# Performance work log

Hardware: AMD Instinct MI355X
Metric: run time of the kernel (lower is better)

## Reference

```python
import jax, jax.numpy as jnp
import numpy as np

B, E_DIM, N_EXP, EXP_SZ, N_TASKS, TOPK = 16384, 512, 16, 512, 2, 3
D_IN = 2 * E_DIM      # 1024
D_HID = 4 * E_DIM     # 2048
EPS = 1e-5


def _ln(x, g, b):
    mu = jnp.mean(x, axis=-1, keepdims=True)
    var = jnp.var(x, axis=-1, keepdims=True)
    return (x - mu) * jax.lax.rsqrt(var + EPS) * g + b


def setup_inputs() -> dict:
    key = jax.random.key(0)
    ks = jax.random.split(key, 24)
    def w(k, shape, fan_in):
        return jax.random.normal(k, shape, jnp.float32) * (1.0 / np.sqrt(fan_in))
    return {
        "emb_paper": jax.random.normal(ks[0], (B, E_DIM), jnp.float32),
        "emb_reviewer": jax.random.normal(ks[1], (B, E_DIM), jnp.float32),
        # interaction encoder
        "enc_W1": w(ks[2], (D_IN, D_HID), D_IN), "enc_b1": jnp.zeros((D_HID,), jnp.float32),
        "ln1_g": jnp.ones((D_HID,), jnp.float32), "ln1_b": jnp.zeros((D_HID,), jnp.float32),
        "enc_W2": w(ks[3], (D_HID, D_IN), D_HID), "enc_b2": jnp.zeros((D_IN,), jnp.float32),
        "ln2_g": jnp.ones((D_IN,), jnp.float32), "ln2_b": jnp.zeros((D_IN,), jnp.float32),
        # per-task gates (stacked over task axis)
        "gW1": w(ks[4], (N_TASKS, D_IN, 128), D_IN), "gb1": jnp.zeros((N_TASKS, 128), jnp.float32),
        "gW2": w(ks[5], (N_TASKS, 128, N_EXP), 128), "gb2": jnp.zeros((N_TASKS, N_EXP), jnp.float32),
        # stacked experts
        "We1": w(ks[6], (N_EXP, D_IN, EXP_SZ), D_IN), "be1": jnp.zeros((N_EXP, EXP_SZ), jnp.float32),
        "We2": w(ks[7], (N_EXP, EXP_SZ, EXP_SZ), EXP_SZ), "be2": jnp.zeros((N_EXP, EXP_SZ), jnp.float32),
        # per-task towers
        "tW1": w(ks[8], (N_TASKS, EXP_SZ, 256), EXP_SZ), "tb1": jnp.zeros((N_TASKS, 256), jnp.float32),
        "tW2": w(ks[9], (N_TASKS, 256, 128), 256), "tb2": jnp.zeros((N_TASKS, 128), jnp.float32),
        "tW3": w(ks[10], (N_TASKS, 128, 1), 128), "tb3": jnp.zeros((N_TASKS, 1), jnp.float32),
        "task_idx": 0,
    }


def reference(emb_paper, emb_reviewer, enc_W1, enc_b1, ln1_g, ln1_b, enc_W2, enc_b2,
              ln2_g, ln2_b, gW1, gb1, gW2, gb2, We1, be1, We2, be2,
              tW1, tb1, tW2, tb2, tW3, tb3, task_idx):
    # interaction encoder (eval mode: dropout is identity)
    x = jnp.concatenate([emb_paper, emb_reviewer], axis=-1)          # [B, 2E]
    h = jax.nn.relu(_ln(x @ enc_W1 + enc_b1, ln1_g, ln1_b))          # [B, 4E]
    feat = _ln(h @ enc_W2 + enc_b2, ln2_g, ln2_b)                    # [B, 2E]

    # task gate -> top-k sparse softmax gates (no router noise in eval)
    g = jax.nn.relu(feat @ gW1[task_idx] + gb1[task_idx])
    logits = g @ gW2[task_idx] + gb2[task_idx]                       # [B, E]
    top_s, top_i = jax.lax.top_k(logits, TOPK)                       # [B, k]
    gates = jnp.zeros_like(logits).at[jnp.arange(logits.shape[0])[:, None], top_i].set(
        jax.nn.softmax(top_s, axis=-1))

    # dense expert stack (faithful to original: all experts computed)
    e1 = jax.nn.relu(jnp.einsum('bi,eio->beo', feat, We1) + be1[None])   # [B, E, S]
    eo = jnp.einsum('beo,eoh->beh', e1, We2) + be2[None]                 # [B, E, S]
    mix = jnp.einsum('be,beh->bh', gates, eo)                            # [B, S]

    # task tower
    t = jax.nn.relu(mix @ tW1[task_idx] + tb1[task_idx])
    t = jax.nn.relu(t @ tW2[task_idx] + tb2[task_idx])
    out = jax.nn.sigmoid(t @ tW3[task_idx] + tb3[task_idx]).squeeze(-1)  # [B]
    return out, task_idx, gates
```

## Files before the change

### kernel.cpp

```cpp
#include <hip/hip_runtime.h>

typedef __attribute__((ext_vector_type(8))) _Float16 f16x8;
typedef __attribute__((ext_vector_type(4))) float f32x4;

#define DEVINL __device__ __forceinline__

constexpr int BATCH = 16384;
constexpr int DIN   = 1024;
constexpr int DHID  = 2048;
constexpr int NEXP  = 16;
constexpr int EXPSZ = 512;
constexpr int NPAIR = BATCH * 3;

DEVINL unsigned short f2h(float v) {
  _Float16 h = (_Float16)v;
  return __builtin_bit_cast(unsigned short, h);
}
DEVINL float h2f(unsigned short u) {
  return (float)__builtin_bit_cast(_Float16, u);
}

DEVINL void gl2lds(const unsigned short* src, char* ldst) {
  __builtin_amdgcn_global_load_lds((const __attribute__((address_space(1))) void*)src,
                                   (__attribute__((address_space(3))) void*)ldst, 16, 0, 0);
}

template<int SPLIT, int AMODE, int EPI, int BK, int NYT, int TASK>
__global__ __launch_bounds__(256, SPLIT ? 2 : 3)
void mgemm_k(const unsigned short* __restrict__ A0p,
             const unsigned short* __restrict__ A1p,
             const unsigned short* __restrict__ B0p,
             const unsigned short* __restrict__ B1p,
             const float* __restrict__ biasb,
             float* __restrict__ Cf, unsigned short* __restrict__ Cb0,
             unsigned short* __restrict__ Cb1,
             const int* __restrict__ pairRow, const float* __restrict__ pairW,
             const int* __restrict__ counts, const int* __restrict__ offs,
             const int* __restrict__ taskPtr,
             int M, int N, int K)
{
  constexpr int KG = BK / 8;
  constexpr int UNITS = 128 * KG;
  constexpr int ISS = UNITS / 256;
  constexpr int NKK = BK / 32;
  constexpr int NARR = SPLIT ? 4 : 2;
  constexpr bool EXPERT = (AMODE == 1 || AMODE == 2);
  __shared__ char smem[NARR * UNITS * 16];
  char* sA0 = smem;
  char* sA1 = smem + UNITS * 16;
  char* sB0 = smem + (SPLIT ? 2 : 1) * UNITS * 16;
  char* sB1 = smem + 3 * UNITS * 16;

  int Mloc = M, rowBase = 0;
  const unsigned short* b0 = B0p;
  const unsigned short* b1 = B1p;
  const float* bias = biasb;
  if (EXPERT) {
    const int e = blockIdx.z;
    Mloc = counts[e];
    rowBase = offs[e];
    const size_t eo = (size_t)e * (size_t)K * N;
    b0 = B0p + eo;
    if (SPLIT) b1 = B1p + eo;
    bias = biasb + (size_t)e * N;
  }
  if (TASK) bias = biasb + (size_t)(*taskPtr) * N;

  const int xcd = (int)blockIdx.x & 7;
  const int j   = (int)blockIdx.x >> 3;
  const int tile0 = (xcd + 8 * (j / NYT)) * 128;
  const int col0  = (j % NYT) * 128;
  if (tile0 >= Mloc) return;

  const int tid = threadIdx.x;
  const int lane = tid & 63;
  const int wr = ((tid >> 6) >> 1) * 64;
  const int wc = ((tid >> 6) & 1) * 64;
  const int l15 = lane & 15;
  const int lg = lane >> 4;

  const int srow = tid & 127;
  size_t aoff;
  if (AMODE == 0) {
    aoff = (size_t)(tile0 + srow) * K;
  } else if (AMODE == 1) {
    int p = rowBase + tile0 + srow; p = p < NPAIR - 1 ? p : NPAIR - 1;
    aoff = (size_t)pairRow[p] * K;
  } else {
    int p = rowBase + tile0 + srow; p = p < NPAIR - 1 ? p : NPAIR - 1;
    aoff = (size_t)p * K;
  }
  const size_t boff = (size_t)(col0 + srow) * K;

  f32x4 acc[4][4];
  f32x4 acc2[4][4];
  #pragma unroll
  for (int m = 0; m < 4; ++m)
    #pragma unroll
    for (int n = 0; n < 4; ++n) {
      acc[m][n] = f32x4{0.f, 0.f, 0.f, 0.f};
      if (SPLIT) acc2[m][n] = f32x4{0.f, 0.f, 0.f, 0.f};
    }

  for (int kt = 0; kt < K; kt += BK) {
    #pragma unroll
    for (int it = 0; it < ISS; ++it) {
      const int uo = (it * 256 + (tid & 192)) * 16;
      const int ko = kt + (it * 2 + (tid >> 7)) * 8;
      gl2lds(A0p + aoff + ko, sA0 + uo);
      if (SPLIT) gl2lds(A1p + aoff + ko, sA1 + uo);
      gl2lds(b0 + boff + ko, sB0 + uo);
      if (SPLIT) gl2lds(b1 + boff + ko, sB1 + uo);
    }
    __syncthreads();
    #pragma unroll
    for (int kk = 0; kk < NKK; ++kk) {
      const int g = kk * 4 + lg;
      f16x8 b0f[4], b1f[4];
      #pragma unroll
      for (int n = 0; n < 4; ++n) {
        const size_t off = (size_t)(g * 128 + wc + n * 16 + l15) * 16;
        b0f[n] = *(const f16x8*)(sB0 + off);
        if (SPLIT) b1f[n] = *(const f16x8*)(sB1 + off);
      }
      #pragma unroll
      for (int m = 0; m < 4; ++m) {
        const size_t ao = (size_t)(g * 128 + wr + m * 16 + l15) * 16;
        const f16x8 a0 = *(const f16x8*)(sA0 + ao);
        f16x8 a1;
        if (SPLIT) a1 = *(const f16x8*)(sA1 + ao);
        #pragma unroll
        for (int n = 0; n < 4; ++n) {
          if (SPLIT) {
            acc2[m][n] = __builtin_amdgcn_mfma_f32_16x16x32_f16(a1, b0f[n], acc2[m][n], 0, 0, 0);
            acc2[m][n] = __builtin_amdgcn_mfma_f32_16x16x32_f16(a0, b1f[n], acc2[m][n], 0, 0, 0);
          }
          acc[m][n] = __builtin_amdgcn_mfma_f32_16x16x32_f16(a0, b0f[n], acc[m][n], 0, 0, 0);
        }
      }
    }
    __syncthreads();
  }

  #pragma unroll
  for (int n = 0; n < 4; ++n) {
    const int cn = col0 + wc + n * 16 + l15;
    const float bv = bias[cn];
    #pragma unroll
    for (int m = 0; m < 4; ++m) {
      const int r0 = wr + m * 16 + ((lane >> 4) << 2);
      #pragma unroll
      for (int jj = 0; jj < 4; ++jj) {
        const int rm = tile0 + r0 + jj;
        if (EXPERT && rm >= Mloc) continue;
        float v = acc[m][n][jj];
        if (SPLIT) v += acc2[m][n][jj] * (1.f / 2048.f);
        v += bv;
        const size_t ci = (size_t)(EXPERT ? (rowBase + rm) : rm) * N + cn;
        if (EPI == 0) {
          const unsigned short h0 = f2h(v);
          Cb0[ci] = h0;
          Cb1[ci] = f2h((v - h2f(h0)) * 2048.f);
        } else if (EPI == 1) {
          Cb0[ci] = f2h(fmaxf(v, 0.f));
        } else if (EPI == 2) {
          Cb0[ci] = f2h(v * pairW[rowBase + rm]);
        } else if (EPI == 3) {
          Cf[ci] = v;
        } else {
          Cf[ci] = fmaxf(v, 0.f);
        }
      }
    }
  }
}

template<int LEV, int TASK>
__global__ __launch_bounds__(256)
void transp_k(const float* __restrict__ src, unsigned short* __restrict__ d0,
              unsigned short* __restrict__ d1, const int* __restrict__ taskPtr,
              int R, int C)
{
  __shared__ float tle[32][33];
  size_t bb = (size_t)blockIdx.z * R * C;
  if (TASK) bb = (size_t)(*taskPtr) * R * C;
  const int r0 = blockIdx.x * 32, c0 = blockIdx.y * 32;
  const int x = threadIdx.x & 31, y = threadIdx.x >> 5;
  #pragma unroll
  for (int i = 0; i < 32; i += 8)
    tle[y + i][x] = src[bb + (size_t)(r0 + y + i) * C + (c0 + x)];
  __syncthreads();
  const size_t db = TASK ? 0 : (size_t)blockIdx.z * R * C;
  #pragma unroll
  for (int i = 0; i < 32; i += 8) {
    const float v = tle[x][y + i];
    const size_t di = db + (size_t)(c0 + y + i) * R + (r0 + x);
    const unsigned short h0 = f2h(v);
    d0[di] = h0;
    if (LEV > 1) d1[di] = f2h((v - h2f(h0)) * 2048.f);
  }
}

__global__ __launch_bounds__(256)
void convx_k(const float* __restrict__ eP, const float* __restrict__ eR,
             unsigned short* __restrict__ x0, unsigned short* __restrict__ x1)
{
  const size_t u = (size_t)blockIdx.x * 256 + threadIdx.x;
  const size_t row = u >> 8;
  const int c4 = (int)(u & 255) * 4;
  const float* s = (c4 < 512) ? (eP + row * 512 + c4) : (eR + row * 512 + (c4 - 512));
  const float4 v = *(const float4*)s;
  const float vv[4] = {v.x, v.y, v.z, v.w};
  ushort4 h4, l4;
  unsigned short* hp = (unsigned short*)&h4;
  unsigned short* lp = (unsigned short*)&l4;
  #pragma unroll
  for (int j = 0; j < 4; ++j) {
    const unsigned short h0 = f2h(vv[j]);
    hp[j] = h0;
    lp[j] = f2h((vv[j] - h2f(h0)) * 2048.f);
  }
  *(ushort4*)(x0 + row * 1024 + c4) = h4;
  *(ushort4*)(x1 + row * 1024 + c4) = l4;
}

template<int COLS, bool RELU>
__global__ __launch_bounds__(256)
void ln_pair_k(unsigned short* __restrict__ h0, unsigned short* __restrict__ h1,
               const float* __restrict__ g, const float* __restrict__ b)
{
  constexpr int PER = COLS / 256;
  const size_t row = blockIdx.x;
  unsigned short* r0 = h0 + row * COLS;
  unsigned short* r1 = h1 + row * COLS;
  const int c0 = threadIdx.x * PER;
  float v[PER];
  float s = 0.f, s2 = 0.f;
  #pragma unroll
  for (int i = 0; i < PER; i += 4) {
    const ushort4 a = *(const ushort4*)(r0 + c0 + i);
    const ushort4 c = *(const ushort4*)(r1 + c0 + i);
    v[i+0] = h2f(a.x) + h2f(c.x) * (1.f/2048.f);
    v[i+1] = h2f(a.y) + h2f(c.y) * (1.f/2048.f);
    v[i+2] = h2f(a.z) + h2f(c.z) * (1.f/2048.f);
    v[i+3] = h2f(a.w) + h2f(c.w) * (1.f/2048.f);
  }
  #pragma unroll
  for (int i = 0; i < PER; ++i) { s += v[i]; s2 += v[i] * v[i]; }
  #pragma unroll
  for (int o = 1; o < 64; o <<= 1) { s += __shfl_xor(s, o); s2 += __shfl_xor(s2, o); }
  __shared__ float ss[4], ss2[4];
  const int w = threadIdx.x >> 6;
  if ((threadIdx.x & 63) == 0) { ss[w] = s; ss2[w] = s2; }
  __syncthreads();
  s  = ss[0] + ss[1] + ss[2] + ss[3];
  s2 = ss2[0] + ss2[1] + ss2[2] + ss2[3];
  const float mu = s * (1.f / COLS);
  const float var = s2 * (1.f / COLS) - mu * mu;
  const float rs = rsqrtf(var + 1e-5f);
  #pragma unroll
  for (int i = 0; i < PER; i += 4) {
    ushort4 a4, c4v;
    unsigned short* ap = (unsigned short*)&a4;
    unsigned short* cp = (unsigned short*)&c4v;
    #pragma unroll
    for (int jq = 0; jq < 4; ++jq) {
      const int c = c0 + i + jq;
      float y = (v[i+jq] - mu) * rs * g[c] + b[c];
      if (RELU) y = fmaxf(y, 0.f);
      const unsigned short hh = f2h(y);
      ap[jq] = hh;
      cp[jq] = f2h((y - h2f(hh)) * 2048.f);
    }
    *(ushort4*)(r0 + c0 + i) = a4;
    *(ushort4*)(r1 + c0 + i) = c4v;
  }
}

__global__ __launch_bounds__(256)
void gate_topk_k(const float* __restrict__ g, const float* __restrict__ gW2,
                 const float* __restrict__ gb2, const int* __restrict__ taskPtr,
                 float* __restrict__ gatesOut, int* __restrict__ topkIdx,
                 float* __restrict__ topkW)
{
  const int t = *taskPtr;
  const float* W = gW2 + (size_t)t * 128 * 16;
  const float* bias = gb2 + (size_t)t * 16;
  const int lane = threadIdx.x & 63;
  const int row = blockIdx.x * 4 + (threadIdx.x >> 6);
  const float* gr = g + (size_t)row * 128;
  const int e = lane & 15;
  const int q = lane >> 4;
  float s = 0.f;
  for (int j = q * 32; j < q * 32 + 32; ++j) s = fmaf(gr[j], W[j * 16 + e], s);
  s += __shfl_xor(s, 16);
  s += __shfl_xor(s, 32);
  s += bias[e];
  float logits[16];
  #pragma unroll
  for (int i = 0; i < 16; ++i) logits[i] = __shfl(s, i);
  int i0 = 0; float v0 = logits[0];
  #pragma unroll
  for (int i = 1; i < 16; ++i) if (logits[i] > v0) { v0 = logits[i]; i0 = i; }
  int i1 = -1; float v1 = -3.4e38f;
  #pragma unroll
  for (int i = 0; i < 16; ++i) if (i != i0 && logits[i] > v1) { v1 = logits[i]; i1 = i; }
  int i2 = -1; float v2 = -3.4e38f;
  #pragma unroll
  for (int i = 0; i < 16; ++i) if (i != i0 && i != i1 && logits[i] > v2) { v2 = logits[i]; i2 = i; }
  const float ex1 = expf(v1 - v0);
  const float ex2 = expf(v2 - v0);
  const float inv = 1.f / (1.f + ex1 + ex2);
  const float p0 = inv, p1 = ex1 * inv, p2 = ex2 * inv;
  if (lane < 16) {
    const float gv = (lane == i0) ? p0 : (lane == i1) ? p1 : (lane == i2) ? p2 : 0.f;
    gatesOut[(size_t)row * 16 + lane] = gv;
  }
  if (lane == 0) {
    topkIdx[row * 3 + 0] = i0; topkIdx[row * 3 + 1] = i1; topkIdx[row * 3 + 2] = i2;
    topkW [row * 3 + 0] = p0; topkW [row * 3 + 1] = p1; topkW [row * 3 + 2] = p2;
  }
}

__global__ __launch_bounds__(256)
void hist_k(const int* __restrict__ topkIdx, int* __restrict__ chunkCnt)
{
  __shared__ int lc[NEXP];
  if (threadIdx.x < NEXP) lc[threadIdx.x] = 0;
  __syncthreads();
  const int row = blockIdx.x * 256 + threadIdx.x;
  #pragma unroll
  for (int k = 0; k < 3; ++k) atomicAdd(&lc[topkIdx[row * 3 + k]], 1);
  __syncthreads();
  if (threadIdx.x < NEXP) chunkCnt[blockIdx.x * NEXP + threadIdx.x] = lc[threadIdx.x];
}

__global__ void scanB_k(const int* __restrict__ chunkCnt, int* __restrict__ counts,
                        int* __restrict__ offs, int* __restrict__ chunkBase)
{
  if (threadIdx.x == 0) {
    int tot[NEXP];
    for (int e = 0; e < NEXP; ++e) tot[e] = 0;
    for (int c = 0; c < 64; ++c)
      for (int e = 0; e < NEXP; ++e) tot[e] += chunkCnt[c * NEXP + e];
    int a = 0;
    for (int e = 0; e < NEXP; ++e) { offs[e] = a; counts[e] = tot[e]; a += tot[e]; }
    for (int e = 0; e < NEXP; ++e) {
      int b = offs[e];
      for (int c = 0; c < 64; ++c) { chunkBase[c * NEXP + e] = b; b += chunkCnt[c * NEXP + e]; }
    }
  }
}

__global__ __launch_bounds__(256)
void fill2_k(const int* __restrict__ topkIdx, const float* __restrict__ topkW,
             const int* __restrict__ chunkBase, int* __restrict__ pairRow,
             float* __restrict__ pairW, int* __restrict__ rowPos)
{
  __shared__ int lc[NEXP];
  if (threadIdx.x < NEXP) lc[threadIdx.x] = 0;
  __syncthreads();
  const int row = blockIdx.x * 256 + threadIdx.x;
  #pragma unroll
  for (int k = 0; k < 3; ++k) {
    const int e = topkIdx[row * 3 + k];
    const int lofs = atomicAdd(&lc[e], 1);
    const int pos = chunkBase[blockIdx.x * NEXP + e] + lofs;
    pairRow[pos] = row;
    pairW[pos] = topkW[row * 3 + k];
    rowPos[row * 3 + k] = pos;
  }
}

__global__ __launch_bounds__(256)
void mixreduce_k(const unsigned short* __restrict__ eo, const int* __restrict__ rowPos,
                 unsigned short* __restrict__ mix16)
{
  const size_t row = blockIdx.x;
  const size_t p0 = rowPos[row * 3 + 0];
  const size_t p1 = rowPos[row * 3 + 1];
  const size_t p2 = rowPos[row * 3 + 2];
  for (int c = threadIdx.x; c < EXPSZ; c += 256) {
    mix16[row * EXPSZ + c] = f2h(h2f(eo[p0 * EXPSZ + c]) + h2f(eo[p1 * EXPSZ + c])
                               + h2f(eo[p2 * EXPSZ + c]));
  }
}

__global__ __launch_bounds__(256)
void tower3_k(const unsigned short* __restrict__ t2, const float* __restrict__ tW3,
              const float* __restrict__ tb3, const int* __restrict__ taskPtr,
              float* __restrict__ out)
{
  const int t = *taskPtr;
  const float* w = tW3 + (size_t)t * 128;
  const float bias = tb3[t];
  const int lane = threadIdx.x & 63;
  const int row = blockIdx.x * 4 + (threadIdx.x >> 6);
  const unsigned short* x = t2 + (size_t)row * 128;
  float s = fmaf(h2f(x[lane]), w[lane], h2f(x[lane + 64]) * w[lane + 64]);
  #pragma unroll
  for (int o = 1; o < 64; o <<= 1) s += __shfl_xor(s, o);
  if (lane == 0) out[row] = 1.f / (1.f + expf(-(s + bias)));
  if (blockIdx.x == 0 && threadIdx.x == 0) out[BATCH] = (float)t;
}

extern "C" void kernel_launch(void* const* d_in, const int* in_sizes, int n_in,
                              void* d_out, int out_size, void* d_ws, size_t ws_size,
                              hipStream_t stream)
{
  (void)in_sizes; (void)n_in; (void)out_size; (void)ws_size;
  const float* embP  = (const float*)d_in[0];
  const float* embR  = (const float*)d_in[1];
  const float* encW1 = (const float*)d_in[2];
  const float* encB1 = (const float*)d_in[3];
  const float* ln1g  = (const float*)d_in[4];
  const float* ln1b  = (const float*)d_in[5];
  const float* encW2 = (const float*)d_in[6];
  const float* encB2 = (const float*)d_in[7];
  const float* ln2g  = (const float*)d_in[8];
  const float* ln2b  = (const float*)d_in[9];
  const float* gW1   = (const float*)d_in[10];
  const float* gb1   = (const float*)d_in[11];
  const float* gW2   = (const float*)d_in[12];
  const float* gb2   = (const float*)d_in[13];
  const float* We1   = (const float*)d_in[14];
  const float* be1   = (const float*)d_in[15];
  const float* We2   = (const float*)d_in[16];
  const float* be2   = (const float*)d_in[17];
  const float* tW1   = (const float*)d_in[18];
  const float* tb1   = (const float*)d_in[19];
  const float* tW2   = (const float*)d_in[20];
  const float* tb2   = (const float*)d_in[21];
  const float* tW3   = (const float*)d_in[22];
  const float* tb3   = (const float*)d_in[23];
  const int* taskPtr = (const int*)d_in[24];

  float* out = (float*)d_out;
  char* ws = (char*)d_ws;
  const size_t MB = 1ull << 20;

  unsigned short* x0    = (unsigned short*)(ws);
  unsigned short* x1    = (unsigned short*)(ws + 32 * MB);
  unsigned short* feat0 = (unsigned short*)(ws);
  unsigned short* feat1 = (unsigned short*)(ws + 32 * MB);
  unsigned short* mix16 = (unsigned short*)(ws + 32 * MB);
  unsigned short* t1f16 = (unsigned short*)(ws + 48 * MB);
  unsigned short* t2f16 = (unsigned short*)(ws + 56 * MB);
  unsigned short* h0    = (unsigned short*)(ws + 64 * MB);
  unsigned short* h1    = (unsigned short*)(ws + 128 * MB);
  unsigned short* We1t0 = (unsigned short*)(ws + 64 * MB);
  unsigned short* We2t0 = (unsigned short*)(ws + 80 * MB);
  unsigned short* e1b   = (unsigned short*)(ws + 88 * MB);
  unsigned short* eob   = (unsigned short*)(ws + 136 * MB);
  unsigned short* W1t0  = (unsigned short*)(ws + 192 * MB);
  unsigned short* W1t1  = (unsigned short*)(ws + 196 * MB);
  unsigned short* W2t0  = (unsigned short*)(ws + 200 * MB);
  unsigned short* W2t1  = (unsigned short*)(ws + 204 * MB);
  unsigned short* gW1t0 = (unsigned short*)(ws + 200 * MB);
  unsigned short* gW1t1 = (unsigned short*)(ws + 204 * MB);
  float* gbuf = (float*)(ws + 192 * MB);
  unsigned short* tW1t = (unsigned short*)(ws + 192 * MB);
  unsigned short* tW2t = (unsigned short*)(ws + 193 * MB);
  char* small = ws + 208 * MB;
  int*   counts    = (int*)  (small);
  int*   offs      = (int*)  (small + 1024);
  int*   chunkCnt  = (int*)  (small + 2048);
  int*   chunkBase = (int*)  (small + 2048 + 4096);
  int*   topkIdx   = (int*)  (small + 16384);
  float* topkW     = (float*)(small + 16384 + 196608);
  int*   pairRow   = (int*)  (small + 16384 + 2 * 196608);
  float* pairW     = (float*)(small + 16384 + 3 * 196608);
  int*   rowPos    = (int*)  (small + 16384 + 4 * 196608);

  const dim3 blk(256, 1, 1);

  convx_k<<<dim3(16384, 1, 1), blk, 0, stream>>>(embP, embR, x0, x1);
  transp_k<2,0><<<dim3(DIN/32, DHID/32, 1), blk, 0, stream>>>(encW1, W1t0, W1t1, nullptr, DIN, DHID);
  mgemm_k<1,0,0,64,DHID/128,0><<<dim3((BATCH/128)*(DHID/128), 1, 1), blk, 0, stream>>>(
      x0, x1, W1t0, W1t1, encB1, nullptr, h0, h1,
      nullptr, nullptr, nullptr, nullptr, nullptr, BATCH, DHID, DIN);
  ln_pair_k<DHID, true><<<dim3(BATCH, 1, 1), blk, 0, stream>>>(h0, h1, ln1g, ln1b);

  transp_k<2,0><<<dim3(DHID/32, DIN/32, 1), blk, 0, stream>>>(encW2, W2t0, W2t1, nullptr, DHID, DIN);
  mgemm_k<1,0,0,64,DIN/128,0><<<dim3((BATCH/128)*(DIN/128), 1, 1), blk, 0, stream>>>(
      h0, h1, W2t0, W2t1, encB2, nullptr, feat0, feat1,
      nullptr, nullptr, nullptr, nullptr, nullptr, BATCH, DIN, DHID);
  ln_pair_k<DIN, false><<<dim3(BATCH, 1, 1), blk, 0, stream>>>(feat0, feat1, ln2g, ln2b);

  transp_k<2,1><<<dim3(DIN/32, 128/32, 1), blk, 0, stream>>>(gW1, gW1t0, gW1t1, taskPtr, DIN, 128);
  mgemm_k<1,0,4,64,1,1><<<dim3(BATCH/128, 1, 1), blk, 0, stream>>>(
      feat0, feat1, gW1t0, gW1t1, gb1, gbuf, nullptr, nullptr,
      nullptr, nullptr, nullptr, nullptr, taskPtr, BATCH, 128, DIN);
  gate_topk_k<<<dim3(BATCH/4, 1, 1), blk, 0, stream>>>(
      gbuf, gW2, gb2, taskPtr, out + BATCH + 1, topkIdx, topkW);
  hist_k<<<dim3(BATCH/256, 1, 1), blk, 0, stream>>>(topkIdx, chunkCnt);
  scanB_k<<<dim3(1, 1, 1), dim3(64, 1, 1), 0, stream>>>(chunkCnt, counts, offs, chunkBase);
  fill2_k<<<dim3(BATCH/256, 1, 1), blk, 0, stream>>>(topkIdx, topkW, chunkBase,
                                                     pairRow, pairW, rowPos);

  transp_k<1,0><<<dim3(DIN/32, EXPSZ/32, NEXP), blk, 0, stream>>>(We1, We1t0, nullptr, nullptr, DIN, EXPSZ);
  transp_k<1,0><<<dim3(EXPSZ/32, EXPSZ/32, NEXP), blk, 0, stream>>>(We2, We2t0, nullptr, nullptr, EXPSZ, EXPSZ);

  mgemm_k<0,1,1,64,EXPSZ/128,0><<<dim3((BATCH/128)*(EXPSZ/128), 1, NEXP), blk, 0, stream>>>(
      feat0, nullptr, We1t0, nullptr, be1, nullptr, e1b, nullptr,
      pairRow, nullptr, counts, offs, nullptr, NPAIR, EXPSZ, DIN);
  mgemm_k<0,2,2,64,EXPSZ/128,0><<<dim3((BATCH/128)*(EXPSZ/128), 1, NEXP), blk, 0, stream>>>(
      e1b, nullptr, We2t0, nullptr, be2, nullptr, eob, nullptr,
      nullptr, pairW, counts, offs, nullptr, NPAIR, EXPSZ, EXPSZ);
  mixreduce_k<<<dim3(BATCH, 1, 1), blk, 0, stream>>>(eob, rowPos, mix16);

  transp_k<1,1><<<dim3(EXPSZ/32, 256/32, 1), blk, 0, stream>>>(tW1, tW1t, nullptr, taskPtr, EXPSZ, 256);
  transp_k<1,1><<<dim3(256/32, 128/32, 1), blk, 0, stream>>>(tW2, tW2t, nullptr, taskPtr, 256, 128);
  mgemm_k<0,0,1,64,2,1><<<dim3((BATCH/128)*2, 1, 1), blk, 0, stream>>>(
      mix16, nullptr, tW1t, nullptr, tb1, nullptr, t1f16, nullptr,
      nullptr, nullptr, nullptr, nullptr, taskPtr, BATCH, 256, EXPSZ);
  mgemm_k<0,0,1,64,1,1><<<dim3(BATCH/128, 1, 1), blk, 0, stream>>>(
      t1f16, nullptr, tW2t, nullptr, tb2, nullptr, t2f16, nullptr,
      nullptr, nullptr, nullptr, nullptr, taskPtr, BATCH, 128, 256);
  tower3_k<<<dim3(BATCH/4, 1, 1), blk, 0, stream>>>(t2f16, tW3, tb3, taskPtr, out);
}
```

Before: 1.173 ms.

## Fuse fp32-to-split-fp16 conversion of GEMM A operands into encoder GEMM loads

```diff
diff --git a/kernel.cpp b/kernel.cpp
--- a/kernel.cpp
+++ b/kernel.cpp
@@ -25,10 +25,11 @@
                                    (__attribute__((address_space(3))) void*)ldst, 16, 0, 0);
 }
 
-template<int SPLIT, int AMODE, int EPI, int BK, int NYT, int TASK>
+template<int SPLIT, int ASTAGE, int AMODE, int EPI, int BK, int NYT, int TASK>
 __global__ __launch_bounds__(256, SPLIT ? 2 : 3)
 void mgemm_k(const unsigned short* __restrict__ A0p,
              const unsigned short* __restrict__ A1p,
+             const float* __restrict__ Af0, const float* __restrict__ Af1,
              const unsigned short* __restrict__ B0p,
              const unsigned short* __restrict__ B1p,
              const float* __restrict__ biasb,
@@ -80,8 +81,18 @@
   const int lg = lane >> 4;
 
   const int srow = tid & 127;
-  size_t aoff;
-  if (AMODE == 0) {
+  size_t aoff = 0;
+  const float* aF = nullptr;
+  const float* aP = nullptr;
+  const float* aR = nullptr;
+  if (ASTAGE) {
+    if (AMODE == 3) {
+      aP = Af0 + (size_t)(tile0 + srow) * 512;
+      aR = Af1 + (size_t)(tile0 + srow) * 512;
+    } else {
+      aF = Af0 + (size_t)(tile0 + srow) * K;
+    }
+  } else if (AMODE == 0) {
     aoff = (size_t)(tile0 + srow) * K;
   } else if (AMODE == 1) {
     int p = rowBase + tile0 + srow; p = p < NPAIR - 1 ? p : NPAIR - 1;
@@ -103,12 +114,36 @@
     }
 
   for (int kt = 0; kt < K; kt += BK) {
+    if (ASTAGE) {
+      #pragma unroll
+      for (int it = 0; it < ISS; ++it) {
+        const int u = it * 256 + tid;
+        const int ko = kt + (u >> 7) * 8;
+        const float* s;
+        if (AMODE == 3) s = (ko < 512) ? (aP + ko) : (aR + (ko - 512));
+        else            s = aF + ko;
+        const float4 x0 = *(const float4*)s;
+        const float4 x1 = *(const float4*)(s + 4);
+        const float vv[8] = {x0.x, x0.y, x0.z, x0.w, x1.x, x1.y, x1.z, x1.w};
+        f16x8 q0, q1;
+        #pragma unroll
+        for (int jq = 0; jq < 8; ++jq) {
+          const _Float16 c0 = (_Float16)vv[jq];
+          q0[jq] = c0;
+          if (SPLIT) q1[jq] = (_Float16)((vv[jq] - (float)c0) * 2048.f);
+        }
+        *(f16x8*)(sA0 + (size_t)u * 16) = q0;
+        if (SPLIT) *(f16x8*)(sA1 + (size_t)u * 16) = q1;
+      }
+    }
     #pragma unroll
     for (int it = 0; it < ISS; ++it) {
       const int uo = (it * 256 + (tid & 192)) * 16;
       const int ko = kt + (it * 2 + (tid >> 7)) * 8;
-      gl2lds(A0p + aoff + ko, sA0 + uo);
-      if (SPLIT) gl2lds(A1p + aoff + ko, sA1 + uo);
+      if (!ASTAGE) {
+        gl2lds(A0p + aoff + ko, sA0 + uo);
+        if (SPLIT) gl2lds(A1p + aoff + ko, sA1 + uo);
+      }
       gl2lds(b0 + boff + ko, sB0 + uo);
       if (SPLIT) gl2lds(b1 + boff + ko, sB1 + uo);
     }
@@ -201,27 +236,39 @@
   }
 }
 
-__global__ __launch_bounds__(256)
-void convx_k(const float* __restrict__ eP, const float* __restrict__ eR,
-             unsigned short* __restrict__ x0, unsigned short* __restrict__ x1)
-{
-  const size_t u = (size_t)blockIdx.x * 256 + threadIdx.x;
-  const size_t row = u >> 8;
-  const int c4 = (int)(u & 255) * 4;
-  const float* s = (c4 < 512) ? (eP + row * 512 + c4) : (eR + row * 512 + (c4 - 512));
-  const float4 v = *(const float4*)s;
-  const float vv[4] = {v.x, v.y, v.z, v.w};
-  ushort4 h4, l4;
-  unsigned short* hp = (unsigned short*)&h4;
-  unsigned short* lp = (unsigned short*)&l4;
-  #pragma unroll
-  for (int j = 0; j < 4; ++j) {
-    const unsigned short h0 = f2h(vv[j]);
-    hp[j] = h0;
-    lp[j] = f2h((vv[j] - h2f(h0)) * 2048.f);
-  }
-  *(ushort4*)(x0 + row * 1024 + c4) = h4;
-  *(ushort4*)(x1 + row * 1024 + c4) = l4;
+template<int COLS, bool RELU>
+__global__ __launch_bounds__(256)
+void ln_k(float* __restrict__ x, const float* __restrict__ g, const float* __restrict__ b)
+{
+  constexpr int PER = COLS / 256;
+  const size_t row = blockIdx.x;
+  float* xr = x + row * COLS;
+  float v[PER];
+  float s = 0.f, s2 = 0.f;
+  #pragma unroll
+  for (int i = 0; i < PER; ++i) {
+    v[i] = xr[threadIdx.x + i * 256];
+    s += v[i];
+    s2 += v[i] * v[i];
+  }
+  #pragma unroll
+  for (int o = 1; o < 64; o <<= 1) { s += __shfl_xor(s, o); s2 += __shfl_xor(s2, o); }
+  __shared__ float ss[4], ss2[4];
+  const int w = threadIdx.x >> 6;
+  if ((threadIdx.x & 63) == 0) { ss[w] = s; ss2[w] = s2; }
+  __syncthreads();
+  s  = ss[0] + ss[1] + ss[2] + ss[3];
+  s2 = ss2[0] + ss2[1] + ss2[2] + ss2[3];
+  const float mu = s * (1.f / COLS);
+  const float var = s2 * (1.f / COLS) - mu * mu;
+  const float rs = rsqrtf(var + 1e-5f);
+  #pragma unroll
+  for (int i = 0; i < PER; ++i) {
+    const int c = threadIdx.x + i * 256;
+    float y = (v[i] - mu) * rs * g[c] + b[c];
+    if (RELU) y = fmaxf(y, 0.f);
+    xr[c] = y;
+  }
 }
 
 template<int COLS, bool RELU>
@@ -439,15 +486,12 @@
   char* ws = (char*)d_ws;
   const size_t MB = 1ull << 20;
 
-  unsigned short* x0    = (unsigned short*)(ws);
-  unsigned short* x1    = (unsigned short*)(ws + 32 * MB);
   unsigned short* feat0 = (unsigned short*)(ws);
   unsigned short* feat1 = (unsigned short*)(ws + 32 * MB);
   unsigned short* mix16 = (unsigned short*)(ws + 32 * MB);
   unsigned short* t1f16 = (unsigned short*)(ws + 48 * MB);
   unsigned short* t2f16 = (unsigned short*)(ws + 56 * MB);
-  unsigned short* h0    = (unsigned short*)(ws + 64 * MB);
-  unsigned short* h1    = (unsigned short*)(ws + 128 * MB);
+  float* h = (float*)(ws + 64 * MB);
   unsigned short* We1t0 = (unsigned short*)(ws + 64 * MB);
   unsigned short* We2t0 = (unsigned short*)(ws + 80 * MB);
   unsigned short* e1b   = (unsigned short*)(ws + 88 * MB);
@@ -474,22 +518,21 @@
 
   const dim3 blk(256, 1, 1);
 
-  convx_k<<<dim3(16384, 1, 1), blk, 0, stream>>>(embP, embR, x0, x1);
   transp_k<2,0><<<dim3(DIN/32, DHID/32, 1), blk, 0, stream>>>(encW1, W1t0, W1t1, nullptr, DIN, DHID);
-  mgemm_k<1,0,0,64,DHID/128,0><<<dim3((BATCH/128)*(DHID/128), 1, 1), blk, 0, stream>>>(
-      x0, x1, W1t0, W1t1, encB1, nullptr, h0, h1,
+  mgemm_k<1,1,3,3,32,DHID/128,0><<<dim3((BATCH/128)*(DHID/128), 1, 1), blk, 0, stream>>>(
+      nullptr, nullptr, embP, embR, W1t0, W1t1, encB1, h, nullptr, nullptr,
       nullptr, nullptr, nullptr, nullptr, nullptr, BATCH, DHID, DIN);
-  ln_pair_k<DHID, true><<<dim3(BATCH, 1, 1), blk, 0, stream>>>(h0, h1, ln1g, ln1b);
+  ln_k<DHID, true><<<dim3(BATCH, 1, 1), blk, 0, stream>>>(h, ln1g, ln1b);
 
   transp_k<2,0><<<dim3(DHID/32, DIN/32, 1), blk, 0, stream>>>(encW2, W2t0, W2t1, nullptr, DHID, DIN);
-  mgemm_k<1,0,0,64,DIN/128,0><<<dim3((BATCH/128)*(DIN/128), 1, 1), blk, 0, stream>>>(
-      h0, h1, W2t0, W2t1, encB2, nullptr, feat0, feat1,
+  mgemm_k<1,1,0,0,32,DIN/128,0><<<dim3((BATCH/128)*(DIN/128), 1, 1), blk, 0, stream>>>(
+      nullptr, nullptr, h, nullptr, W2t0, W2t1, encB2, nullptr, feat0, feat1,
       nullptr, nullptr, nullptr, nullptr, nullptr, BATCH, DIN, DHID);
   ln_pair_k<DIN, false><<<dim3(BATCH, 1, 1), blk, 0, stream>>>(feat0, feat1, ln2g, ln2b);
 
   transp_k<2,1><<<dim3(DIN/32, 128/32, 1), blk, 0, stream>>>(gW1, gW1t0, gW1t1, taskPtr, DIN, 128);
-  mgemm_k<1,0,4,64,1,1><<<dim3(BATCH/128, 1, 1), blk, 0, stream>>>(
-      feat0, feat1, gW1t0, gW1t1, gb1, gbuf, nullptr, nullptr,
+  mgemm_k<1,0,0,4,64,1,1><<<dim3(BATCH/128, 1, 1), blk, 0, stream>>>(
+      feat0, feat1, nullptr, nullptr, gW1t0, gW1t1, gb1, gbuf, nullptr, nullptr,
       nullptr, nullptr, nullptr, nullptr, taskPtr, BATCH, 128, DIN);
   gate_topk_k<<<dim3(BATCH/4, 1, 1), blk, 0, stream>>>(
       gbuf, gW2, gb2, taskPtr, out + BATCH + 1, topkIdx, topkW);
@@ -501,21 +544,21 @@
   transp_k<1,0><<<dim3(DIN/32, EXPSZ/32, NEXP), blk, 0, stream>>>(We1, We1t0, nullptr, nullptr, DIN, EXPSZ);
   transp_k<1,0><<<dim3(EXPSZ/32, EXPSZ/32, NEXP), blk, 0, stream>>>(We2, We2t0, nullptr, nullptr, EXPSZ, EXPSZ);
 
-  mgemm_k<0,1,1,64,EXPSZ/128,0><<<dim3((BATCH/128)*(EXPSZ/128), 1, NEXP), blk, 0, stream>>>(
-      feat0, nullptr, We1t0, nullptr, be1, nullptr, e1b, nullptr,
+  mgemm_k<0,0,1,1,64,EXPSZ/128,0><<<dim3((BATCH/128)*(EXPSZ/128), 1, NEXP), blk, 0, stream>>>(
+      feat0, nullptr, nullptr, nullptr, We1t0, nullptr, be1, nullptr, e1b, nullptr,
       pairRow, nullptr, counts, offs, nullptr, NPAIR, EXPSZ, DIN);
-  mgemm_k<0,2,2,64,EXPSZ/128,0><<<dim3((BATCH/128)*(EXPSZ/128), 1, NEXP), blk, 0, stream>>>(
-      e1b, nullptr, We2t0, nullptr, be2, nullptr, eob, nullptr,
+  mgemm_k<0,0,2,2,64,EXPSZ/128,0><<<dim3((BATCH/128)*(EXPSZ/128), 1, NEXP), blk, 0, stream>>>(
+      e1b, nullptr, nullptr, nullptr, We2t0, nullptr, be2, nullptr, eob, nullptr,
       nullptr, pairW, counts, offs, nullptr, NPAIR, EXPSZ, EXPSZ);
   mixreduce_k<<<dim3(BATCH, 1, 1), blk, 0, stream>>>(eob, rowPos, mix16);
 
   transp_k<1,1><<<dim3(EXPSZ/32, 256/32, 1), blk, 0, stream>>>(tW1, tW1t, nullptr, taskPtr, EXPSZ, 256);
   transp_k<1,1><<<dim3(256/32, 128/32, 1), blk, 0, stream>>>(tW2, tW2t, nullptr, taskPtr, 256, 128);
-  mgemm_k<0,0,1,64,2,1><<<dim3((BATCH/128)*2, 1, 1), blk, 0, stream>>>(
-      mix16, nullptr, tW1t, nullptr, tb1, nullptr, t1f16, nullptr,
+  mgemm_k<0,0,0,1,64,2,1><<<dim3((BATCH/128)*2, 1, 1), blk, 0, stream>>>(
+      mix16, nullptr, nullptr, nullptr, tW1t, nullptr, tb1, nullptr, t1f16, nullptr,
       nullptr, nullptr, nullptr, nullptr, taskPtr, BATCH, 256, EXPSZ);
-  mgemm_k<0,0,1,64,1,1><<<dim3(BATCH/128, 1, 1), blk, 0, stream>>>(
-      t1f16, nullptr, tW2t, nullptr, tb2, nullptr, t2f16, nullptr,
+  mgemm_k<0,0,0,1,64,1,1><<<dim3(BATCH/128, 1, 1), blk, 0, stream>>>(
+      t1f16, nullptr, nullptr, nullptr, tW2t, nullptr, tb2, nullptr, t2f16, nullptr,
       nullptr, nullptr, nullptr, nullptr, taskPtr, BATCH, 128, 256);
   tower3_k<<<dim3(BATCH/4, 1, 1), blk, 0, stream>>>(t2f16, tW3, tb3, taskPtr, out);
 }
```

Measured after the change: 1.110 ms. 1.06x faster.
